# Kernel optimization log

Hardware: AMD Instinct MI355X
Metric: run time of the kernel (lower is better)

The kernel has to match this reference:

```python
import jax, jax.numpy as jnp
import numpy as np

BUCKET_BINS = np.array([0, 1, 2, 3, 4, 5, 7, 8, 15, 16, 31, 32, 63, 64], dtype=np.int32)
MAX_WINDOW = 8  # args.span_maximum_length


def _span_index_table(L):
    # Static enumeration of all spans of width 1..MAX_WINDOW (stride-1 unfold).
    starts, ends = [], []
    for w in range(1, min(L, MAX_WINDOW) + 1):
        s = np.arange(0, L - w + 1)
        starts.append(s)
        ends.append(s + w)
    return (np.concatenate(starts).astype(np.int32),
            np.concatenate(ends).astype(np.int32))


def _bucket(width):
    # index of last bin with width >= bin value
    return jnp.searchsorted(jnp.asarray(BUCKET_BINS), width, side='right') - 1


def _fnn(h, W1, b1, W2, b2, W3, b3):
    # Linear->ReLU->(Dropout: eval identity)->Linear->ReLU->Linear->Softmax
    h = jax.nn.relu(h @ W1 + b1)
    h = jax.nn.relu(h @ W2 + b2)
    return jax.nn.softmax(h @ W3 + b3, axis=-1)


def setup_inputs() -> dict:
    key = jax.random.key(0)
    ks = jax.random.split(key, 16)
    B, L, D = 8, 256, 768
    H, WD, DD = 1024, 25, 25
    span_dim = 2 * D + WD          # 1561
    pair_dim = 2 * span_dim + DD   # 3147
    f = jnp.float32

    def g(k, shape, scale):
        return jax.random.normal(k, shape, dtype=f) * scale

    return {
        'x': g(ks[0], (B, L, D), 1.0),
        'width_emb': g(ks[1], (len(BUCKET_BINS), WD), 0.02),
        'dist_emb': g(ks[2], (len(BUCKET_BINS), DD), 0.02),
        'Ws1': g(ks[3], (span_dim, H), 0.02), 'bs1': jnp.zeros((H,), f),
        'Ws2': g(ks[4], (H, H), 0.02), 'bs2': jnp.zeros((H,), f),
        'Ws3': g(ks[5], (H, 3), 0.02), 'bs3': jnp.zeros((3,), f),
        'Wp1': g(ks[6], (pair_dim, H), 0.02), 'bp1': jnp.zeros((H,), f),
        'Wp2': g(ks[7], (H, H), 0.02), 'bp2': jnp.zeros((H,), f),
        'Wp3': g(ks[8], (H, 4), 0.02), 'bp3': jnp.zeros((4,), f),
        'nz': 64,
    }


def reference(x, width_emb, dist_emb, Ws1, bs1, Ws2, bs2, Ws3, bs3,
              Wp1, bp1, Wp2, bp2, Wp3, bp3, nz):
    B, L, D = x.shape
    starts_np, ends_np = _span_index_table(L)
    starts = jnp.asarray(starts_np)
    ends = jnp.asarray(ends_np)

    # ---- SpanRepresentation: [start token, end token, width bucket emb] ----
    w_emb = width_emb[_bucket(ends - starts)]                     # [S, WD]
    spans = jnp.concatenate([
        x[:, starts_np, :],                                       # [B,S,D]
        x[:, ends_np - 1, :],                                     # [B,S,D]
        jnp.broadcast_to(w_emb, (B,) + w_emb.shape),              # [B,S,WD]
    ], axis=-1)                                                   # [B,S,span_dim]

    # ---- span_fnn + PrunedTargetOpinion (top-k on aspect/opinion probs) ----
    span_prob = _fnn(spans, Ws1, bs1, Ws2, bs2, Ws3, bs3)         # [B,S,3]
    _, t_idx = jax.lax.top_k(span_prob[:, :, 1], nz)              # aspect  [B,nz]
    _, o_idx = jax.lax.top_k(span_prob[:, :, 2], nz)              # opinion [B,nz]

    # ---- PairRepresentation: all target x opinion pairs ----
    t_rep = jnp.take_along_axis(spans, t_idx[:, :, None], axis=1) # [B,nz,sd]
    o_rep = jnp.take_along_axis(spans, o_idx[:, :, None], axis=1)
    ta, tb = starts[t_idx], ends[t_idx]                           # [B,nz]
    oc, od = starts[o_idx], ends[o_idx]
    # min_distance(a,b,c,d) = min(|b-c|, |a-d|)
    dist = jnp.minimum(jnp.abs(tb[:, :, None] - oc[:, None, :]),
                       jnp.abs(ta[:, :, None] - od[:, None, :]))  # [B,nz,nz]
    d_emb = dist_emb[_bucket(dist)]                               # [B,nz,nz,DD]
    sd = spans.shape[-1]
    pairs = jnp.concatenate([
        jnp.broadcast_to(t_rep[:, :, None, :], (B, nz, nz, sd)),
        jnp.broadcast_to(o_rep[:, None, :, :], (B, nz, nz, sd)),
        d_emb,
    ], axis=-1).reshape(B, nz * nz, 2 * sd + d_emb.shape[-1])     # [B,nz^2,pair_dim]

    pair_prob = _fnn(pairs, Wp1, bp1, Wp2, bp2, Wp3, bp3)         # [B,nz^2,4]
    return span_prob, pair_prob
```

## Files before the change

kernel.cpp:

```cpp
#include <hip/hip_runtime.h>
#include <cstdint>
#include <cstddef>

#define BATCH 8
#define SEQ   256
#define DIM   768
#define NSPAN 2020
#define HID   1024
#define NZ    64

typedef unsigned short u16;
typedef unsigned int   u32;
typedef unsigned long long u64;

typedef __bf16 bf16x8 __attribute__((ext_vector_type(8)));
typedef float  f32x4  __attribute__((ext_vector_type(4)));

__device__ __forceinline__ u16 f2bf(float f) {
    union { float f; u32 u; } x; x.f = f;
    u32 r = x.u + 0x7fffu + ((x.u >> 16) & 1u);
    return (u16)(r >> 16);
}
__device__ __forceinline__ float bf2f(u16 b) {
    union { u32 u; float f; } x; x.u = ((u32)b) << 16;
    return x.f;
}
__device__ __forceinline__ void splitbf(float v, u16& h, u16& l) {
    h = f2bf(v);
    l = f2bf(v - bf2f(h));
}

__device__ __forceinline__ void gld_lds16(const void* g, void* l) {
    __builtin_amdgcn_global_load_lds(
        (const __attribute__((address_space(1))) unsigned int*)g,
        (__attribute__((address_space(3))) unsigned int*)l, 16, 0, 0);
}

__device__ __forceinline__ void span_decode(int s, int& start, int& end, int& w) {
    int off = 0;
#pragma unroll
    for (int wi = 1; wi <= 8; ++wi) {
        int cnt = SEQ - wi + 1;
        if (s < off + cnt) { w = wi; start = s - off; end = start + wi; return; }
        off += cnt;
    }
    w = 8; start = 0; end = 8;
}

__device__ __forceinline__ int dbucket(int d) {
    int b = 0;
    b += (d >= 1);  b += (d >= 2);  b += (d >= 3);  b += (d >= 4);
    b += (d >= 5);  b += (d >= 7);  b += (d >= 8);  b += (d >= 15);
    b += (d >= 16); b += (d >= 31); b += (d >= 32); b += (d >= 63);
    b += (d >= 64);
    return b;
}

__device__ __forceinline__ void xcd_map(int L, int sft, int& bx, int& by) {
    int grp = L >> (3 + sft);
    int rem = L & ((1 << (3 + sft)) - 1);
    bx = rem >> 3;
    by = (grp << 3) | (rem & 7);
}

__global__ __launch_bounds__(256) void k_prep(
    const float* __restrict__ x,  u16* __restrict__ xh,   u16* __restrict__ xl,
    const float* __restrict__ wemb, const float* __restrict__ demb,
    const float* __restrict__ bs1, const float* __restrict__ bp1,
    float* __restrict__ wtabS, float* __restrict__ wtabPt,
    float* __restrict__ wtabPo, float* __restrict__ dtab,
    const float* __restrict__ Ws1, u16* __restrict__ W1Th, u16* __restrict__ W1Tl,
    const float* __restrict__ Ws2, u16* __restrict__ W2Th, u16* __restrict__ W2Tl,
    const float* __restrict__ Wp2, u16* __restrict__ Wp2T,
    const float* __restrict__ Wp1, u16* __restrict__ Wp1T4)
{
    __shared__ float tile[32][33];
    const int bid = blockIdx.x, tid = threadIdx.x;
    if (bid < 6144) {
        int i = bid * 256 + tid;
        u16 h, l; splitbf(x[i], h, l);
        xh[i] = h; xl[i] = l;
        return;
    }
    if (bid < 6296) {
        int t = bid - 6144;
        int row = t >> 2;
        int h = (t & 3) * 256 + tid;
        const int wb[8] = {1,2,3,4,5,5,6,7};
        if (row < 8) {
            int bk = wb[row];
            float acc = bs1[h];
            for (int j = 0; j < 25; ++j) acc = fmaf(wemb[bk*25+j], Ws1[(size_t)(1536+j)*HID + h], acc);
            wtabS[row*HID + h] = acc;
        } else if (row < 16) {
            int bk = wb[row-8];
            float acc = 0.f;
            for (int j = 0; j < 25; ++j) acc = fmaf(wemb[bk*25+j], Wp1[(size_t)(1536+j)*HID + h], acc);
            wtabPt[(row-8)*HID + h] = acc;
        } else if (row < 24) {
            int bk = wb[row-16];
            float acc = 0.f;
            for (int j = 0; j < 25; ++j) acc = fmaf(wemb[bk*25+j], Wp1[(size_t)(3097+j)*HID + h], acc);
            wtabPo[(row-16)*HID + h] = acc;
        } else {
            int tt = row - 24;
            float acc = bp1[h];
            for (int j = 0; j < 25; ++j) acc = fmaf(demb[tt*25+j], Wp1[(size_t)(3122+j)*HID + h], acc);
            dtab[tt*HID + h] = acc;
        }
        return;
    }
    const int tb = bid - 6296;
    const int tr = tid >> 3;
    const int tc4 = (tid & 7) * 4;
    int job, tk, tn, blk = 0;
    if (tb < 1536)      { job = 0; tk = tb % 24; tn = tb / 24; }
    else if (tb < 2560) { job = 1; int t = tb - 1536; tk = t & 31; tn = t >> 5; }
    else if (tb < 3584) { job = 2; int t = tb - 2560; tk = t & 31; tn = t >> 5; }
    else                { job = 3; int t = tb - 3584; blk = t / 768; int r = t - blk * 768; tk = r % 24; tn = r / 24; }
    const int k0 = tk * 32, n0 = tn * 32;

    int k = k0 + tr;
    float4 v;
    if (job == 0) {
        const float* s = (n0 < 1024) ? (Ws1 + (size_t)k * HID + n0)
                                     : (Ws1 + (size_t)(768 + k) * HID + (n0 - 1024));
        v = *(const float4*)(s + tc4);
    } else if (job == 1) {
        v = *(const float4*)(Ws2 + (size_t)k * HID + n0 + tc4);
    } else if (job == 2) {
        v = *(const float4*)(Wp2 + (size_t)k * HID + n0 + tc4);
    } else {
        const int roff[4] = {0, 768, 1561, 2329};
        v = *(const float4*)(Wp1 + (size_t)(roff[blk] + k) * HID + n0 + tc4);
    }
    tile[tr][tc4+0] = v.x; tile[tr][tc4+1] = v.y;
    tile[tr][tc4+2] = v.z; tile[tr][tc4+3] = v.w;
    __syncthreads();

    int nn = n0 + tr;
    float w0 = tile[tc4+0][tr], w1 = tile[tc4+1][tr];
    float w2 = tile[tc4+2][tr], w3 = tile[tc4+3][tr];
    if (job == 0) {
        size_t d = (size_t)nn * 768 + k0 + tc4;
        u16 h0,l0,h1,l1,h2,l2,h3,l3;
        splitbf(w0,h0,l0); splitbf(w1,h1,l1); splitbf(w2,h2,l2); splitbf(w3,h3,l3);
        *(uint2*)(W1Th + d) = make_uint2((u32)h0 | ((u32)h1 << 16), (u32)h2 | ((u32)h3 << 16));
        *(uint2*)(W1Tl + d) = make_uint2((u32)l0 | ((u32)l1 << 16), (u32)l2 | ((u32)l3 << 16));
    } else if (job == 1) {
        size_t d = (size_t)nn * 1024 + k0 + tc4;
        u16 h0,l0,h1,l1,h2,l2,h3,l3;
        splitbf(w0,h0,l0); splitbf(w1,h1,l1); splitbf(w2,h2,l2); splitbf(w3,h3,l3);
        *(uint2*)(W2Th + d) = make_uint2((u32)h0 | ((u32)h1 << 16), (u32)h2 | ((u32)h3 << 16));
        *(uint2*)(W2Tl + d) = make_uint2((u32)l0 | ((u32)l1 << 16), (u32)l2 | ((u32)l3 << 16));
    } else if (job == 2) {
        size_t d = (size_t)nn * 1024 + k0 + tc4;
        *(uint2*)(Wp2T + d) = make_uint2((u32)f2bf(w0) | ((u32)f2bf(w1) << 16),
                                         (u32)f2bf(w2) | ((u32)f2bf(w3) << 16));
    } else {
        size_t d = (size_t)blk * 786432 + (size_t)nn * 768 + k0 + tc4;
        *(uint2*)(Wp1T4 + d) = make_uint2((u32)f2bf(w0) | ((u32)f2bf(w1) << 16),
                                          (u32)f2bf(w2) | ((u32)f2bf(w3) << 16));
    }
}

__global__ __launch_bounds__(256) void k_gemm3bf(
    const u16* __restrict__ Ah, const u16* __restrict__ Al, int lda,
    const u16* __restrict__ BTh, const u16* __restrict__ BTl, int ldb,
    float* __restrict__ C, int ldc,
    int M, int K, int nby, int sft)
{
    int bx, by;
    xcd_map(blockIdx.x, sft, bx, by);
    if (by >= nby) return;
    __shared__ __align__(16) u16 sm[4 * 128 * 32];
    u16* sAh = sm;
    u16* sAl = sm + 4096;
    u16* sBh = sm + 8192;
    u16* sBl = sm + 12288;
    const int tid = threadIdx.x;
    const int bm = by * 128, bn = bx * 128;
    const int wave = tid >> 6, lane = tid & 63;
    const int wr = wave >> 1, wc = wave & 1;
    const int q = lane >> 4, tl = lane & 15;

    f32x4 zero = {0.f, 0.f, 0.f, 0.f};
    f32x4 acc[4][4];
#pragma unroll
    for (int i = 0; i < 4; ++i)
#pragma unroll
        for (int j = 0; j < 4; ++j) acc[i][j] = zero;

    const int srow = lane >> 2;
    const int scol = (lane & 3) * 8;
    int ra0 = bm + wave * 32 + srow;      if (ra0 >= M) ra0 = M - 1;
    int ra1 = bm + wave * 32 + 16 + srow; if (ra1 >= M) ra1 = M - 1;
    const int rb0 = bn + wave * 32 + srow;
    const int rb1 = bn + wave * 32 + 16 + srow;
    u16* dA0 = sAh + wave * 1024;  u16* dA1 = dA0 + 512;
    u16* dL0 = sAl + wave * 1024;  u16* dL1 = dL0 + 512;
    u16* dB0 = sBh + wave * 1024;  u16* dB1 = dB0 + 512;
    u16* dC0 = sBl + wave * 1024;  u16* dC1 = dC0 + 512;
    const u16* gA0 = Ah  + (size_t)ra0 * lda + scol;
    const u16* gA1 = Ah  + (size_t)ra1 * lda + scol;
    const u16* gL0 = Al  + (size_t)ra0 * lda + scol;
    const u16* gL1 = Al  + (size_t)ra1 * lda + scol;
    const u16* gB0 = BTh + (size_t)rb0 * ldb + scol;
    const u16* gB1 = BTh + (size_t)rb1 * ldb + scol;
    const u16* gC0 = BTl + (size_t)rb0 * ldb + scol;
    const u16* gC1 = BTl + (size_t)rb1 * ldb + scol;

    for (int k0 = 0; k0 < K; k0 += 32) {
        gld_lds16(gA0 + k0, dA0);
        gld_lds16(gA1 + k0, dA1);
        gld_lds16(gL0 + k0, dL0);
        gld_lds16(gL1 + k0, dL1);
        gld_lds16(gB0 + k0, dB0);
        gld_lds16(gB1 + k0, dB1);
        gld_lds16(gC0 + k0, dC0);
        gld_lds16(gC1 + k0, dC1);
        __syncthreads();
        bf16x8 ah[4], al[4], bh[4], bl[4];
#pragma unroll
        for (int t = 0; t < 4; ++t) {
            int arow = (wr*64 + t*16 + tl) * 32 + q*8;
            int brow = (wc*64 + t*16 + tl) * 32 + q*8;
            ah[t] = *(const bf16x8*)(&sAh[arow]);
            al[t] = *(const bf16x8*)(&sAl[arow]);
            bh[t] = *(const bf16x8*)(&sBh[brow]);
            bl[t] = *(const bf16x8*)(&sBl[brow]);
        }
#pragma unroll
        for (int ti = 0; ti < 4; ++ti)
#pragma unroll
            for (int tj = 0; tj < 4; ++tj) {
                acc[ti][tj] = __builtin_amdgcn_mfma_f32_16x16x32_bf16(ah[ti], bh[tj], acc[ti][tj], 0, 0, 0);
                acc[ti][tj] = __builtin_amdgcn_mfma_f32_16x16x32_bf16(al[ti], bh[tj], acc[ti][tj], 0, 0, 0);
                acc[ti][tj] = __builtin_amdgcn_mfma_f32_16x16x32_bf16(ah[ti], bl[tj], acc[ti][tj], 0, 0, 0);
            }
        __syncthreads();
    }
#pragma unroll
    for (int ti = 0; ti < 4; ++ti) {
#pragma unroll
        for (int tj = 0; tj < 4; ++tj) {
            int gcol = bn + wc*64 + tj*16 + tl;
#pragma unroll
            for (int r = 0; r < 4; ++r) {
                int grow = bm + wr*64 + ti*16 + q*4 + r;
                if (grow >= M) continue;
                C[(size_t)grow * ldc + gcol] = acc[ti][tj][r];
            }
        }
    }
}

#define MFB __builtin_amdgcn_mfma_f32_16x16x32_bf16
#define MFROW(i, A, B) \
    acc[i][0] = MFB(A, B[0], acc[i][0], 0, 0, 0); \
    acc[i][1] = MFB(A, B[1], acc[i][1], 0, 0, 0); \
    acc[i][2] = MFB(A, B[2], acc[i][2], 0, 0, 0); \
    acc[i][3] = MFB(A, B[3], acc[i][3], 0, 0, 0);

#define SPAN_PHASE(P, VMC) \
    { \
        bf16x8 ah0 = *(const bf16x8*)(smr + rA + (2*(P)+0)*512); \
        bf16x8 ah1 = *(const bf16x8*)(smr + rA + (2*(P)+1)*512); \
        bf16x8 al0 = *(const bf16x8*)(smr + rA + 8192 + (2*(P)+0)*512); \
        bf16x8 al1 = *(const bf16x8*)(smr + rA + 8192 + (2*(P)+1)*512); \
        if ((P) == 0) { \
            bh[0] = *(const bf16x8*)(smr + rB + 0*512); \
            bh[1] = *(const bf16x8*)(smr + rB + 1*512); \
            bh[2] = *(const bf16x8*)(smr + rB + 2*512); \
            bh[3] = *(const bf16x8*)(smr + rB + 3*512); \
            bl[0] = *(const bf16x8*)(smr + rB + 8192 + 0*512); \
            bl[1] = *(const bf16x8*)(smr + rB + 8192 + 1*512); \
            bl[2] = *(const bf16x8*)(smr + rB + 8192 + 2*512); \
            bl[3] = *(const bf16x8*)(smr + rB + 8192 + 3*512); \
        } \
        gld_lds16(gsrc[2*(P)+0] + kn, smw + ldst[2*(P)+0]); \
        gld_lds16(gsrc[2*(P)+1] + kn, smw + ldst[2*(P)+1]); \
        asm volatile("s_waitcnt vmcnt(" #VMC ")" ::: "memory"); \
        asm volatile("s_barrier" ::: "memory"); \
        __builtin_amdgcn_sched_barrier(0); \
        __builtin_amdgcn_s_setprio(1); \
        MFROW(2*(P)+0, ah0, bh) \
        MFROW(2*(P)+1, ah1, bh) \
        MFROW(2*(P)+0, al0, bh) \
        MFROW(2*(P)+1, al1, bh) \
        MFROW(2*(P)+0, ah0, bl) \
        MFROW(2*(P)+1, ah1, bl) \
        __builtin_amdgcn_s_setprio(0); \
        asm volatile("s_barrier" ::: "memory"); \
    }

__global__ __launch_bounds__(512, 2) void k_span_l2(
    const u16* __restrict__ Ah, const u16* __restrict__ Al,
    const u16* __restrict__ BTh, const u16* __restrict__ BTl,
    const float* __restrict__ bs2, const float* __restrict__ Ws3,
    float* __restrict__ part, int M)
{
    __shared__ __align__(16) u16 sm[65536];
    const int tid = threadIdx.x;
    const int swz = (blockIdx.x & 7) * 32 + (blockIdx.x >> 3);
    const int by = swz >> 2, bx = swz & 3;
    const int bm = by * 256, bn = bx * 256;
    const int wave = tid >> 6, lane = tid & 63;
    const int wm = wave >> 2, wn = wave & 3;
    const int tl = lane & 15, q8 = lane >> 4;

    const int sr  = lane >> 2;
    const int scs = lane & 3;
    const int scl = scs ^ ((sr >> 1) & 3);
    const u16* gsrc[8];
    u32 ldst[8];
#pragma unroll
    for (int c = 0; c < 4; ++c) {
        int arr  = 2 + (c >> 1);
        int half = c & 1;
        int sb   = wave;
        int row  = bn + half * 128 + sb * 16 + sr;
        const u16* base = (arr == 2) ? BTh : BTl;
        gsrc[c] = base + (size_t)row * HID + scl * 8;
        ldst[c] = arr * 8192 + half * 4096 + sb * 512;
    }
#pragma unroll
    for (int p = 0; p < 4; ++p) {
        int arr  = wave >> 2;
        int half = (wave >> 1) & 1;
        int sb   = 2 * p + (wave & 1);
        int row  = bm + half * 128 + sb * 16 + sr;
        if (row >= M) row = M - 1;
        const u16* base = arr ? Al : Ah;
        gsrc[4 + p] = base + (size_t)row * HID + scl * 8;
        ldst[4 + p] = arr * 8192 + half * 4096 + sb * 512;
    }
    const int cpr = q8 ^ ((tl >> 1) & 3);
    const u32 lof = (u32)(tl * 32 + cpr * 8);
    const u32 rA  = (u32)(wm * 4096) + lof;
    const u32 rB  = 16384u + (u32)((wn >> 1) * 4096 + (wn & 1) * 2048) + lof;

    f32x4 zero = {0.f, 0.f, 0.f, 0.f};
    f32x4 acc[8][4];
#pragma unroll
    for (int i = 0; i < 8; ++i)
#pragma unroll
        for (int j = 0; j < 4; ++j) acc[i][j] = zero;

#pragma unroll
    for (int c = 0; c < 8; ++c) gld_lds16(gsrc[c], sm + ldst[c]);
    asm volatile("s_waitcnt vmcnt(3)" ::: "memory");
    asm volatile("s_barrier" ::: "memory");

    bf16x8 bh[4], bl[4];
    for (int t = 0; t < 32; ++t) {
        const u16* smr = sm + ((t & 1) ? 32768u : 0u);
        u16*       smw = sm + ((t & 1) ? 0u : 32768u);
        const int  kn  = (t + 1) * 32;
        SPAN_PHASE(0, 4)
        SPAN_PHASE(1, 5)
        SPAN_PHASE(2, 6)
        SPAN_PHASE(3, 3)
    }

    const int slot = bx * 4 + wn;
#pragma unroll
    for (int fm = 0; fm < 8; ++fm) {
#pragma unroll
        for (int r = 0; r < 4; ++r) {
            int grow = bm + wm * 128 + fm * 16 + q8 * 4 + r;
            float l0 = 0.f, l1 = 0.f, l2 = 0.f;
#pragma unroll
            for (int fn = 0; fn < 4; ++fn) {
                int gcol = bn + wn * 64 + fn * 16 + tl;
                float v = fmaxf(acc[fm][fn][r] + bs2[gcol], 0.f);
                const float* w3 = Ws3 + gcol * 3;
                l0 = fmaf(v, w3[0], l0);
                l1 = fmaf(v, w3[1], l1);
                l2 = fmaf(v, w3[2], l2);
            }
#pragma unroll
            for (int off = 8; off > 0; off >>= 1) {
                l0 += __shfl_down(l0, off, 16);
                l1 += __shfl_down(l1, off, 16);
                l2 += __shfl_down(l2, off, 16);
            }
            if (tl == 0 && grow < M) {
                float* dst = part + ((size_t)grow * 16 + slot) * 3;
                dst[0] = l0; dst[1] = l1; dst[2] = l2;
            }
        }
    }
    asm volatile("s_waitcnt vmcnt(0)" ::: "memory");
}

__global__ __launch_bounds__(256) void k_pairL1(
    const u16* __restrict__ xh, const u16* __restrict__ Wp1T4,
    float* __restrict__ TO2, const int* __restrict__ toks)
{
    __shared__ __align__(16) u16 sm[2 * 64 * 32];
    u16* sA = sm;
    u16* sB = sm + 2048;
    const int tid = threadIdx.x;
    const int bid = blockIdx.x;
    const int p = bid >> 8;
    const int bx = bid & 15, by = (bid >> 4) & 15;
    const int bm = by * 64, bn = bx * 64;
    const int wave = tid >> 6, lane = tid & 63;
    const int wr = wave >> 1, wc = wave & 1;
    const int q = lane >> 4, tl = lane & 15;
    const bool isO = bm >= 512;

    f32x4 zero = {0.f, 0.f, 0.f, 0.f};
    f32x4 acc[2][2];
#pragma unroll
    for (int i = 0; i < 2; ++i)
#pragma unroll
        for (int j = 0; j < 2; ++j) acc[i][j] = zero;

    const int srow = tid >> 2;
    const int scol = (tid & 3) * 8;
    u16* dA = sA + wave * 512;
    u16* dB = sB + wave * 512;

    int arow = toks[bm + srow + p * 1024];
    const u16* gA = xh + (size_t)arow * DIM + scol;
    const u16* gB = Wp1T4 + ((size_t)((isO ? 2 : 0) + p) * 1024 + bn + srow) * DIM + scol;
    for (int k0 = 0; k0 < DIM; k0 += 32) {
        gld_lds16(gA + k0, dA);
        gld_lds16(gB + k0, dB);
        __syncthreads();
        bf16x8 af[2], bf[2];
#pragma unroll
        for (int t = 0; t < 2; ++t) {
            af[t] = *(const bf16x8*)(&sA[(wr*32 + t*16 + tl) * 32 + q*8]);
            bf[t] = *(const bf16x8*)(&sB[(wc*32 + t*16 + tl) * 32 + q*8]);
        }
#pragma unroll
        for (int ti = 0; ti < 2; ++ti)
#pragma unroll
            for (int tj = 0; tj < 2; ++tj)
                acc[ti][tj] = __builtin_amdgcn_mfma_f32_16x16x32_bf16(af[ti], bf[tj], acc[ti][tj], 0, 0, 0);
        __syncthreads();
    }
    float* dstb = TO2 + (size_t)p * 1024 * HID;
#pragma unroll
    for (int ti = 0; ti < 2; ++ti) {
#pragma unroll
        for (int tj = 0; tj < 2; ++tj) {
            int gcol = bn + wc*32 + tj*16 + tl;
#pragma unroll
            for (int r = 0; r < 4; ++r) {
                int grow = bm + wr*32 + ti*16 + q*4 + r;
                dstb[(size_t)grow * HID + gcol] = acc[ti][tj][r];
            }
        }
    }
}

__global__ __launch_bounds__(256) void k_build_h1s(
    const float* __restrict__ XALL, const float* __restrict__ wtabS,
    u16* __restrict__ h1h, u16* __restrict__ h1l)
{
    int r = blockIdx.x;
    int b = r / NSPAN, s = r - b * NSPAN;
    int st, en, w; span_decode(s, st, en, w);
    const float4* xs = (const float4*)(XALL + (size_t)(b*SEQ + st) * 2048);
    const float4* xe = (const float4*)(XALL + (size_t)(b*SEQ + en - 1) * 2048 + 1024);
    const float4* wt = (const float4*)(wtabS + (size_t)(w-1) * HID);
    int t = threadIdx.x;
    float4 a = xs[t], bz = xe[t], c = wt[t];
    float v0 = fmaxf(a.x + bz.x + c.x, 0.f);
    float v1 = fmaxf(a.y + bz.y + c.y, 0.f);
    float v2 = fmaxf(a.z + bz.z + c.z, 0.f);
    float v3 = fmaxf(a.w + bz.w + c.w, 0.f);
    u16 h0,l0,h1,l1,h2,l2,h3,l3;
    splitbf(v0,h0,l0); splitbf(v1,h1,l1); splitbf(v2,h2,l2); splitbf(v3,h3,l3);
    size_t base = (size_t)r * HID + t * 4;
    *(uint2*)(h1h + base) = make_uint2((u32)h0 | ((u32)h1 << 16), (u32)h2 | ((u32)h3 << 16));
    *(uint2*)(h1l + base) = make_uint2((u32)l0 | ((u32)l1 << 16), (u32)l2 | ((u32)l3 << 16));
}

__global__ __launch_bounds__(256) void k_topk(
    const float* __restrict__ partS, const float* __restrict__ bs3,
    float* __restrict__ out, int* __restrict__ t_idx, int* __restrict__ o_idx,
    int* __restrict__ toks)
{
    int b = blockIdx.x >> 1;
    int head = 1 + (blockIdx.x & 1);
    int* outp = (head == 1 ? t_idx : o_idx) + b * NZ;
    __shared__ u64 keys[2048];
    int tid = threadIdx.x;
#pragma unroll
    for (int ii = 0; ii < 8; ++ii) {
        int s = tid + ii * 256;
        u32 fb = 0;
        if (s < NSPAN) {
            const float* p = partS + (size_t)(b * NSPAN + s) * 48;
            float s0 = bs3[0], s1 = bs3[1], s2 = bs3[2];
#pragma unroll
            for (int t = 0; t < 16; ++t) {
                s0 += p[t*3]; s1 += p[t*3+1]; s2 += p[t*3+2];
            }
            float m = fmaxf(s0, fmaxf(s1, s2));
            float e0 = expf(s0 - m), e1 = expf(s1 - m), e2 = expf(s2 - m);
            float inv = 1.f / (e0 + e1 + e2);
            float p0 = e0 * inv, p1 = e1 * inv, p2 = e2 * inv;
            float* o = out + (size_t)(b * NSPAN + s) * 3;
            o[0] = p0; o[1] = p1; o[2] = p2;
            union { float f; u32 u; } x;
            x.f = (head == 1) ? p1 : p2;
            fb = x.u;
        }
        keys[s] = ((u64)fb << 32) | (u64)(0xFFFFFFFFu - (u32)s);
    }
    __syncthreads();
    for (int k = 2; k <= 2048; k <<= 1) {
        for (int j = k >> 1; j > 0; j >>= 1) {
#pragma unroll
            for (int ii = 0; ii < 8; ++ii) {
                int i = tid + ii * 256;
                int ixj = i ^ j;
                if (ixj > i) {
                    u64 a = keys[i], c = keys[ixj];
                    bool desc = (i & k) == 0;
                    bool wrong = desc ? (a < c) : (a > c);
                    if (wrong) { keys[i] = c; keys[ixj] = a; }
                }
            }
            __syncthreads();
        }
    }
    if (tid < NZ) {
        u64 key = keys[tid];
        int fi = (int)(0xFFFFFFFFu - (u32)(key & 0xFFFFFFFFu));
        if (fi < 0 || fi >= NSPAN) fi = 0;
        outp[tid] = fi;
        int st, en, w; span_decode(fi, st, en, w);
        int base = (head == 1 ? 0 : 512) + b * NZ + tid;
        toks[base] = b * SEQ + st;
        toks[1024 + base] = b * SEQ + en - 1;
    }
}

__global__ __launch_bounds__(256) void k_build_h1p(
    const float* __restrict__ TO2, const int* __restrict__ t_idx, const int* __restrict__ o_idx,
    const float* __restrict__ wtabPt, const float* __restrict__ wtabPo,
    const float* __restrict__ dtab, u16* __restrict__ h1p)
{
    __shared__ float Ts[8][HID];
    __shared__ float Os[4][HID];
    const int bid = blockIdx.x;
    const int b = bid >> 7;
    const int it = (bid >> 4) & 7;
    const int jt = bid & 15;
    const int i0 = it * 8, j0 = jt * 4;
    const int tid = threadIdx.x;
    const int k4 = tid * 4;
    const size_t PS = (size_t)1024 * HID;

    int tinfo[8][2];
    int oinfo[4][2];
#pragma unroll
    for (int r = 0; r < 8; ++r) {
        int i = i0 + r;
        int ts = t_idx[b*64 + i];
        int ta, tb, wt; span_decode(ts, ta, tb, wt);
        tinfo[r][0] = ta; tinfo[r][1] = tb;
        float4 t0 = *(const float4*)(TO2 + (size_t)(b*64 + i) * HID + k4);
        float4 t1 = *(const float4*)(TO2 + PS + (size_t)(b*64 + i) * HID + k4);
        float4 pp = *(const float4*)(wtabPt + (size_t)(wt-1) * HID + k4);
        Ts[r][k4+0] = t0.x + t1.x + pp.x;
        Ts[r][k4+1] = t0.y + t1.y + pp.y;
        Ts[r][k4+2] = t0.z + t1.z + pp.z;
        Ts[r][k4+3] = t0.w + t1.w + pp.w;
    }
#pragma unroll
    for (int r = 0; r < 4; ++r) {
        int j = j0 + r;
        int os = o_idx[b*64 + j];
        int oc, od, wo; span_decode(os, oc, od, wo);
        oinfo[r][0] = oc; oinfo[r][1] = od;
        float4 o0 = *(const float4*)(TO2 + (size_t)(512 + b*64 + j) * HID + k4);
        float4 o1 = *(const float4*)(TO2 + PS + (size_t)(512 + b*64 + j) * HID + k4);
        float4 qq = *(const float4*)(wtabPo + (size_t)(wo-1) * HID + k4);
        Os[r][k4+0] = o0.x + o1.x + qq.x;
        Os[r][k4+1] = o0.y + o1.y + qq.y;
        Os[r][k4+2] = o0.z + o1.z + qq.z;
        Os[r][k4+3] = o0.w + o1.w + qq.w;
    }
    __syncthreads();

#pragma unroll
    for (int ri = 0; ri < 8; ++ri) {
#pragma unroll
        for (int rj = 0; rj < 4; ++rj) {
            int ta = tinfo[ri][0], tb = tinfo[ri][1];
            int oc = oinfo[rj][0], od = oinfo[rj][1];
            int d1 = tb - oc; d1 = d1 < 0 ? -d1 : d1;
            int d2 = ta - od; d2 = d2 < 0 ? -d2 : d2;
            int dist = d1 < d2 ? d1 : d2;
            int db = dbucket(dist);
            const float4 dd = *(const float4*)(dtab + (size_t)db * HID + k4);
            float vx = fmaxf(Ts[ri][k4+0] + Os[rj][k4+0] + dd.x, 0.f);
            float vy = fmaxf(Ts[ri][k4+1] + Os[rj][k4+1] + dd.y, 0.f);
            float vz = fmaxf(Ts[ri][k4+2] + Os[rj][k4+2] + dd.z, 0.f);
            float vw = fmaxf(Ts[ri][k4+3] + Os[rj][k4+3] + dd.w, 0.f);
            u32 p0 = (u32)f2bf(vx) | ((u32)f2bf(vy) << 16);
            u32 p1 = (u32)f2bf(vz) | ((u32)f2bf(vw) << 16);
            int row = b * 4096 + (i0 + ri) * 64 + (j0 + rj);
            *(uint2*)(h1p + (size_t)row * HID + k4) = make_uint2(p0, p1);
        }
    }
}

#define PAIR_PHASE(P, VMC) \
    { \
        bf16x8 a00 = *(const bf16x8*)(smr + rA + ((2*(P)+0)*2+0)*512); \
        bf16x8 a01 = *(const bf16x8*)(smr + rA + ((2*(P)+0)*2+1)*512); \
        bf16x8 a10 = *(const bf16x8*)(smr + rA + ((2*(P)+1)*2+0)*512); \
        bf16x8 a11 = *(const bf16x8*)(smr + rA + ((2*(P)+1)*2+1)*512); \
        if ((P) == 0) { \
            b0[0] = *(const bf16x8*)(smr + rB + 0*512); \
            b1[0] = *(const bf16x8*)(smr + rB + 1*512); \
            b0[1] = *(const bf16x8*)(smr + rB + 2*512); \
            b1[1] = *(const bf16x8*)(smr + rB + 3*512); \
            b0[2] = *(const bf16x8*)(smr + rB + 4*512); \
            b1[2] = *(const bf16x8*)(smr + rB + 5*512); \
            b0[3] = *(const bf16x8*)(smr + rB + 6*512); \
            b1[3] = *(const bf16x8*)(smr + rB + 7*512); \
        } \
        gld_lds16(gsrc[2*(P)+0] + kn, smw + ldst[2*(P)+0]); \
        gld_lds16(gsrc[2*(P)+1] + kn, smw + ldst[2*(P)+1]); \
        asm volatile("s_waitcnt vmcnt(" #VMC ")" ::: "memory"); \
        asm volatile("s_barrier" ::: "memory"); \
        __builtin_amdgcn_sched_barrier(0); \
        __builtin_amdgcn_s_setprio(1); \
        MFROW(2*(P)+0, a00, b0) \
        MFROW(2*(P)+1, a10, b0) \
        MFROW(2*(P)+0, a01, b1) \
        MFROW(2*(P)+1, a11, b1) \
        __builtin_amdgcn_s_setprio(0); \
        asm volatile("s_barrier" ::: "memory"); \
    }

__global__ __launch_bounds__(512, 2) void k_pair_l2(
    const u16* __restrict__ Abf, const u16* __restrict__ BT,
    const float* __restrict__ bp2, const float* __restrict__ Wp3,
    float* __restrict__ part)
{
    __shared__ __align__(16) u16 sm[65536];
    const int tid = threadIdx.x;
    const int swz = (blockIdx.x & 7) * 64 + (blockIdx.x >> 3);
    const int by = swz >> 2, bx = swz & 3;
    const int bm = by * 256, bn = bx * 256;
    const int wave = tid >> 6, lane = tid & 63;
    const int wm = wave >> 2, wn = wave & 3;
    const int tl = lane & 15, q8 = lane >> 4;

    const int sr  = lane >> 2;
    const int scs = lane & 3;
    const int scl = scs ^ ((sr >> 1) & 3);
    const u16* gsrc[8];
    u32 ldst[8];
#pragma unroll
    for (int c = 0; c < 4; ++c) {
        int half = c >> 1;
        int sb   = (c & 1) * 8 + wave;
        int row  = bn + half * 128 + (sb >> 1) * 16 + sr;
        gsrc[c] = BT + (size_t)row * HID + (sb & 1) * 32 + scl * 8;
        ldst[c] = 16384 + half * 8192 + sb * 512;
    }
#pragma unroll
    for (int p = 0; p < 4; ++p) {
        int half = wave >> 2;
        int sb   = 4 * p + (wave & 3);
        int row  = bm + half * 128 + (sb >> 1) * 16 + sr;
        gsrc[4 + p] = Abf + (size_t)row * HID + (sb & 1) * 32 + scl * 8;
        ldst[4 + p] = half * 8192 + sb * 512;
    }
    const int cpr = q8 ^ ((tl >> 1) & 3);
    const u32 lof = (u32)(tl * 32 + cpr * 8);
    const u32 rA  = (u32)(wm * 8192) + lof;
    const u32 rB  = 16384u + (u32)((wn >> 1) * 8192 + (wn & 1) * 4096) + lof;

    f32x4 zero = {0.f, 0.f, 0.f, 0.f};
    f32x4 acc[8][4];
#pragma unroll
    for (int i = 0; i < 8; ++i)
#pragma unroll
        for (int j = 0; j < 4; ++j) acc[i][j] = zero;

#pragma unroll
    for (int c = 0; c < 8; ++c) gld_lds16(gsrc[c], sm + ldst[c]);
    asm volatile("s_waitcnt vmcnt(3)" ::: "memory");
    asm volatile("s_barrier" ::: "memory");

    bf16x8 b0[4], b1[4];
    for (int t = 0; t < 16; ++t) {
        const u16* smr = sm + ((t & 1) ? 32768u : 0u);
        u16*       smw = sm + ((t & 1) ? 0u : 32768u);
        const int  kn  = (t + 1) * 64;
        PAIR_PHASE(0, 4)
        PAIR_PHASE(1, 5)
        PAIR_PHASE(2, 6)
        PAIR_PHASE(3, 3)
    }

    const int slot = bx * 4 + wn;
#pragma unroll
    for (int fm = 0; fm < 8; ++fm) {
#pragma unroll
        for (int r = 0; r < 4; ++r) {
            int grow = bm + wm * 128 + fm * 16 + q8 * 4 + r;
            float l0 = 0.f, l1 = 0.f, l2 = 0.f, l3 = 0.f;
#pragma unroll
            for (int fn = 0; fn < 4; ++fn) {
                int gcol = bn + wn * 64 + fn * 16 + tl;
                float v = fmaxf(acc[fm][fn][r] + bp2[gcol], 0.f);
                const float4 w = *(const float4*)(Wp3 + gcol * 4);
                l0 = fmaf(v, w.x, l0); l1 = fmaf(v, w.y, l1);
                l2 = fmaf(v, w.z, l2); l3 = fmaf(v, w.w, l3);
            }
#pragma unroll
            for (int off = 8; off > 0; off >>= 1) {
                l0 += __shfl_down(l0, off, 16);
                l1 += __shfl_down(l1, off, 16);
                l2 += __shfl_down(l2, off, 16);
                l3 += __shfl_down(l3, off, 16);
            }
            if (tl == 0) {
                float* dst = part + ((size_t)grow * 16 + slot) * 4;
                dst[0] = l0; dst[1] = l1; dst[2] = l2; dst[3] = l3;
            }
        }
    }
    asm volatile("s_waitcnt vmcnt(0)" ::: "memory");
}

__global__ __launch_bounds__(256) void k_pair_red(
    const float* __restrict__ part, const float* __restrict__ bp3,
    float* __restrict__ out)
{
    int r = blockIdx.x * 256 + threadIdx.x;
    const float4* p = (const float4*)(part + (size_t)r * 64);
    float s0 = bp3[0], s1 = bp3[1], s2 = bp3[2], s3 = bp3[3];
#pragma unroll
    for (int t = 0; t < 16; ++t) {
        float4 v = p[t];
        s0 += v.x; s1 += v.y; s2 += v.z; s3 += v.w;
    }
    float m = fmaxf(fmaxf(s0, s1), fmaxf(s2, s3));
    float e0 = expf(s0 - m), e1 = expf(s1 - m), e2 = expf(s2 - m), e3 = expf(s3 - m);
    float inv = 1.f / (e0 + e1 + e2 + e3);
    float* o = out + (size_t)r * 4;
    o[0] = e0 * inv; o[1] = e1 * inv; o[2] = e2 * inv; o[3] = e3 * inv;
}

extern "C" void kernel_launch(void* const* d_in, const int* in_sizes, int n_in,
                              void* d_out, int out_size, void* d_ws, size_t ws_size,
                              hipStream_t stream)
{
    const float* x    = (const float*)d_in[0];
    const float* wemb = (const float*)d_in[1];
    const float* demb = (const float*)d_in[2];
    const float* Ws1  = (const float*)d_in[3];
    const float* bs1  = (const float*)d_in[4];
    const float* Ws2  = (const float*)d_in[5];
    const float* bs2  = (const float*)d_in[6];
    const float* Ws3  = (const float*)d_in[7];
    const float* bs3  = (const float*)d_in[8];
    const float* Wp1  = (const float*)d_in[9];
    const float* bp1  = (const float*)d_in[10];
    const float* Wp2  = (const float*)d_in[11];
    const float* bp2  = (const float*)d_in[12];
    const float* Wp3  = (const float*)d_in[13];
    const float* bp3  = (const float*)d_in[14];
    float* out = (float*)d_out;
    char* ws = (char*)d_ws;

    const size_t RSZ = (size_t)32768 * HID * 2;
    size_t off = 0;
    auto alloc = [&](size_t bytes) -> void* {
        void* p = ws + off;
        off += (bytes + 255) & ~(size_t)255;
        return p;
    };
    char* R1 = (char*)alloc(RSZ);
    char* R2 = (char*)alloc(RSZ);
    u16*   h1h  = (u16*)R1;
    u16*   h1l  = (u16*)(R1 + (size_t)16160 * HID * 2);
    float* XALL = (float*)R2;
    u16*   xl   = (u16*)(R2 + (16u << 20));
    u16*   W1Th = (u16*)(R2 + (19u << 20));
    u16*   W1Tl = (u16*)(R2 + (22u << 20));
    u16*   h1p  = (u16*)R2;
    u16*   xh     = (u16*)alloc((size_t)2048 * DIM * 2);
    float* TO2    = (float*)alloc((size_t)2 * 1024 * HID * 4);
    float* partS  = (float*)alloc((size_t)16160 * 16 * 3 * 4);
    float* partP  = (float*)alloc((size_t)32768 * 16 * 4 * 4);
    u16*   W2Th   = (u16*)alloc((size_t)1024 * 1024 * 2);
    u16*   W2Tl   = (u16*)alloc((size_t)1024 * 1024 * 2);
    u16*   Wp2T   = (u16*)alloc((size_t)1024 * 1024 * 2);
    u16*   Wp1T4  = (u16*)alloc((size_t)4 * 1024 * 768 * 2);
    float* wtabS  = (float*)alloc(8 * HID * 4);
    float* wtabPt = (float*)alloc(8 * HID * 4);
    float* wtabPo = (float*)alloc(8 * HID * 4);
    float* dtab   = (float*)alloc(14 * HID * 4);
    int*   t_idx  = (int*)alloc(BATCH * NZ * 4);
    int*   o_idx  = (int*)alloc(BATCH * NZ * 4);
    int*   toks   = (int*)alloc(2048 * 4);
    (void)ws_size; (void)in_sizes; (void)n_in; (void)out_size;

    k_prep<<<12952, 256, 0, stream>>>(x, xh, xl, wemb, demb, bs1, bp1,
                                      wtabS, wtabPt, wtabPo, dtab,
                                      Ws1, W1Th, W1Tl, Ws2, W2Th, W2Tl,
                                      Wp2, Wp2T, Wp1, Wp1T4);

    k_gemm3bf<<<256, 256, 0, stream>>>(xh, xl, 768, W1Th, W1Tl, 768,
                                       XALL, 2048, 2048, 768, 16, 4);
    k_build_h1s<<<16160, 256, 0, stream>>>(XALL, wtabS, h1h, h1l);
    k_span_l2<<<256, 512, 0, stream>>>(h1h, h1l, W2Th, W2Tl, bs2, Ws3, partS, 16160);
    k_topk<<<16, 256, 0, stream>>>(partS, bs3, out, t_idx, o_idx, toks);
    k_pairL1<<<512, 256, 0, stream>>>(xh, Wp1T4, TO2, toks);
    k_build_h1p<<<1024, 256, 0, stream>>>(TO2, t_idx, o_idx, wtabPt, wtabPo, dtab, h1p);
    k_pair_l2<<<512, 512, 0, stream>>>(h1p, Wp2T, bp2, Wp3, partP);
    k_pair_red<<<128, 256, 0, stream>>>(partP, bp3, out + 48480);
}
```

Before: 438.5 us.

## Retile pair layer-2 GEMM to 256x128 tiles and rebalance span prefetch

The pair layer-2 GEMM moves from 256x256 tiles with K-step 64 to 256x128 tiles with K-step 32. Shared memory drops to 48 KB and launch bounds rise to four blocks per CU, doubling the grid to 1024 blocks. The partial-logit buffer grows to 32 slots per row and is aliased into the now-dead R1 region, and the reduction kernel sums 32 partials. The span layer-2 loop redistributes its eight global-to-LDS loads across phases (3/2/2/1) with adjusted vmcnt waits. Smaller tiles trade lower arithmetic intensity per byte loaded for higher occupancy and better latency hiding.

```diff
diff --git a/kernel.cpp b/kernel.cpp
--- a/kernel.cpp
+++ b/kernel.cpp
@@ -261,8 +261,11 @@
     acc[i][1] = MFB(A, B[1], acc[i][1], 0, 0, 0); \
     acc[i][2] = MFB(A, B[2], acc[i][2], 0, 0, 0); \
     acc[i][3] = MFB(A, B[3], acc[i][3], 0, 0, 0);
-
-#define SPAN_PHASE(P, VMC) \
+#define MFROW2(i, A, B) \
+    acc[i][0] = MFB(A, B[0], acc[i][0], 0, 0, 0); \
+    acc[i][1] = MFB(A, B[1], acc[i][1], 0, 0, 0);
+
+#define SPAN_PHASE(P, VMC, GLDS) \
     { \
         bf16x8 ah0 = *(const bf16x8*)(smr + rA + (2*(P)+0)*512); \
         bf16x8 ah1 = *(const bf16x8*)(smr + rA + (2*(P)+1)*512); \
@@ -278,8 +281,7 @@
             bl[2] = *(const bf16x8*)(smr + rB + 8192 + 2*512); \
             bl[3] = *(const bf16x8*)(smr + rB + 8192 + 3*512); \
         } \
-        gld_lds16(gsrc[2*(P)+0] + kn, smw + ldst[2*(P)+0]); \
-        gld_lds16(gsrc[2*(P)+1] + kn, smw + ldst[2*(P)+1]); \
+        GLDS \
         asm volatile("s_waitcnt vmcnt(" #VMC ")" ::: "memory"); \
         asm volatile("s_barrier" ::: "memory"); \
         __builtin_amdgcn_sched_barrier(0); \
@@ -357,10 +359,18 @@
         const u16* smr = sm + ((t & 1) ? 32768u : 0u);
         u16*       smw = sm + ((t & 1) ? 0u : 32768u);
         const int  kn  = (t + 1) * 32;
-        SPAN_PHASE(0, 4)
-        SPAN_PHASE(1, 5)
-        SPAN_PHASE(2, 6)
-        SPAN_PHASE(3, 3)
+        SPAN_PHASE(0, 5,
+            gld_lds16(gsrc[0] + kn, smw + ldst[0]);
+            gld_lds16(gsrc[1] + kn, smw + ldst[1]);
+            gld_lds16(gsrc[2] + kn, smw + ldst[2]);)
+        SPAN_PHASE(1, 6,
+            gld_lds16(gsrc[3] + kn, smw + ldst[3]);
+            gld_lds16(gsrc[4] + kn, smw + ldst[4]);)
+        SPAN_PHASE(2, 7,
+            gld_lds16(gsrc[5] + kn, smw + ldst[5]);
+            gld_lds16(gsrc[6] + kn, smw + ldst[6]);)
+        SPAN_PHASE(3, 3,
+            gld_lds16(gsrc[7] + kn, smw + ldst[7]);)
     }
 
     const int slot = bx * 4 + wn;
@@ -614,46 +624,39 @@
     }
 }
 
-#define PAIR_PHASE(P, VMC) \
+#define PAIR4_PHASE(FM0, VMC, GLDS) \
     { \
-        bf16x8 a00 = *(const bf16x8*)(smr + rA + ((2*(P)+0)*2+0)*512); \
-        bf16x8 a01 = *(const bf16x8*)(smr + rA + ((2*(P)+0)*2+1)*512); \
-        bf16x8 a10 = *(const bf16x8*)(smr + rA + ((2*(P)+1)*2+0)*512); \
-        bf16x8 a11 = *(const bf16x8*)(smr + rA + ((2*(P)+1)*2+1)*512); \
-        if ((P) == 0) { \
-            b0[0] = *(const bf16x8*)(smr + rB + 0*512); \
-            b1[0] = *(const bf16x8*)(smr + rB + 1*512); \
-            b0[1] = *(const bf16x8*)(smr + rB + 2*512); \
-            b1[1] = *(const bf16x8*)(smr + rB + 3*512); \
-            b0[2] = *(const bf16x8*)(smr + rB + 4*512); \
-            b1[2] = *(const bf16x8*)(smr + rB + 5*512); \
-            b0[3] = *(const bf16x8*)(smr + rB + 6*512); \
-            b1[3] = *(const bf16x8*)(smr + rB + 7*512); \
+        bf16x8 a0 = *(const bf16x8*)(smr + rA + ((FM0)+0)*512); \
+        bf16x8 a1 = *(const bf16x8*)(smr + rA + ((FM0)+1)*512); \
+        bf16x8 a2 = *(const bf16x8*)(smr + rA + ((FM0)+2)*512); \
+        bf16x8 a3 = *(const bf16x8*)(smr + rA + ((FM0)+3)*512); \
+        if ((FM0) == 0) { \
+            bb[0] = *(const bf16x8*)(smr + rB + 0*512); \
+            bb[1] = *(const bf16x8*)(smr + rB + 1*512); \
         } \
-        gld_lds16(gsrc[2*(P)+0] + kn, smw + ldst[2*(P)+0]); \
-        gld_lds16(gsrc[2*(P)+1] + kn, smw + ldst[2*(P)+1]); \
+        GLDS \
         asm volatile("s_waitcnt vmcnt(" #VMC ")" ::: "memory"); \
         asm volatile("s_barrier" ::: "memory"); \
         __builtin_amdgcn_sched_barrier(0); \
         __builtin_amdgcn_s_setprio(1); \
-        MFROW(2*(P)+0, a00, b0) \
-        MFROW(2*(P)+1, a10, b0) \
-        MFROW(2*(P)+0, a01, b1) \
-        MFROW(2*(P)+1, a11, b1) \
+        MFROW2((FM0)+0, a0, bb) \
+        MFROW2((FM0)+1, a1, bb) \
+        MFROW2((FM0)+2, a2, bb) \
+        MFROW2((FM0)+3, a3, bb) \
         __builtin_amdgcn_s_setprio(0); \
         asm volatile("s_barrier" ::: "memory"); \
     }
 
-__global__ __launch_bounds__(512, 2) void k_pair_l2(
+__global__ __launch_bounds__(512, 4) void k_pair_l2(
     const u16* __restrict__ Abf, const u16* __restrict__ BT,
     const float* __restrict__ bp2, const float* __restrict__ Wp3,
     float* __restrict__ part)
 {
-    __shared__ __align__(16) u16 sm[65536];
+    __shared__ __align__(16) u16 sm[24576];
     const int tid = threadIdx.x;
-    const int swz = (blockIdx.x & 7) * 64 + (blockIdx.x >> 3);
-    const int by = swz >> 2, bx = swz & 3;
-    const int bm = by * 256, bn = bx * 256;
+    const int swz = (blockIdx.x & 7) * 128 + (blockIdx.x >> 3);
+    const int by = swz >> 3, bx = swz & 7;
+    const int bm = by * 256, bn = bx * 128;
     const int wave = tid >> 6, lane = tid & 63;
     const int wm = wave >> 2, wn = wave & 3;
     const int tl = lane & 15, q8 = lane >> 4;
@@ -661,50 +664,48 @@
     const int sr  = lane >> 2;
     const int scs = lane & 3;
     const int scl = scs ^ ((sr >> 1) & 3);
-    const u16* gsrc[8];
-    u32 ldst[8];
-#pragma unroll
-    for (int c = 0; c < 4; ++c) {
-        int half = c >> 1;
-        int sb   = (c & 1) * 8 + wave;
-        int row  = bn + half * 128 + (sb >> 1) * 16 + sr;
-        gsrc[c] = BT + (size_t)row * HID + (sb & 1) * 32 + scl * 8;
-        ldst[c] = 16384 + half * 8192 + sb * 512;
-    }
-#pragma unroll
-    for (int p = 0; p < 4; ++p) {
-        int half = wave >> 2;
-        int sb   = 4 * p + (wave & 3);
-        int row  = bm + half * 128 + (sb >> 1) * 16 + sr;
-        gsrc[4 + p] = Abf + (size_t)row * HID + (sb & 1) * 32 + scl * 8;
-        ldst[4 + p] = half * 8192 + sb * 512;
+    const u16* gsrc[3];
+    u32 ldst[3];
+    {
+        int rowB = bn + wave * 16 + sr;
+        gsrc[0] = BT + (size_t)rowB * HID + scl * 8;
+        ldst[0] = 8192 + wave * 512;
+        int ps1 = (wave & 3) + (wave >> 2) * 8;
+        int rowA1 = bm + ps1 * 16 + sr;
+        gsrc[1] = Abf + (size_t)rowA1 * HID + scl * 8;
+        ldst[1] = ps1 * 512;
+        int ps2 = ps1 + 4;
+        int rowA2 = bm + ps2 * 16 + sr;
+        gsrc[2] = Abf + (size_t)rowA2 * HID + scl * 8;
+        ldst[2] = ps2 * 512;
     }
     const int cpr = q8 ^ ((tl >> 1) & 3);
     const u32 lof = (u32)(tl * 32 + cpr * 8);
-    const u32 rA  = (u32)(wm * 8192) + lof;
-    const u32 rB  = 16384u + (u32)((wn >> 1) * 8192 + (wn & 1) * 4096) + lof;
+    const u32 rA  = (u32)(wm * 4096) + lof;
+    const u32 rB  = 8192u + (u32)(wn * 1024) + lof;
 
     f32x4 zero = {0.f, 0.f, 0.f, 0.f};
-    f32x4 acc[8][4];
+    f32x4 acc[8][2];
 #pragma unroll
     for (int i = 0; i < 8; ++i)
 #pragma unroll
-        for (int j = 0; j < 4; ++j) acc[i][j] = zero;
-
-#pragma unroll
-    for (int c = 0; c < 8; ++c) gld_lds16(gsrc[c], sm + ldst[c]);
-    asm volatile("s_waitcnt vmcnt(3)" ::: "memory");
+        for (int j = 0; j < 2; ++j) acc[i][j] = zero;
+
+#pragma unroll
+    for (int c = 0; c < 3; ++c) gld_lds16(gsrc[c], sm + ldst[c]);
+    asm volatile("s_waitcnt vmcnt(1)" ::: "memory");
     asm volatile("s_barrier" ::: "memory");
 
-    bf16x8 b0[4], b1[4];
-    for (int t = 0; t < 16; ++t) {
-        const u16* smr = sm + ((t & 1) ? 32768u : 0u);
-        u16*       smw = sm + ((t & 1) ? 0u : 32768u);
-        const int  kn  = (t + 1) * 64;
-        PAIR_PHASE(0, 4)
-        PAIR_PHASE(1, 5)
-        PAIR_PHASE(2, 6)
-        PAIR_PHASE(3, 3)
+    bf16x8 bb[2];
+    for (int t = 0; t < 32; ++t) {
+        const u16* smr = sm + ((t & 1) ? 12288u : 0u);
+        u16*       smw = sm + ((t & 1) ? 0u : 12288u);
+        const int  kn  = (t + 1) * 32;
+        PAIR4_PHASE(0, 2,
+            gld_lds16(gsrc[0] + kn, smw + ldst[0]);
+            gld_lds16(gsrc[1] + kn, smw + ldst[1]);)
+        PAIR4_PHASE(4, 1,
+            gld_lds16(gsrc[2] + kn, smw + ldst[2]);)
     }
 
     const int slot = bx * 4 + wn;
@@ -715,8 +716,8 @@
             int grow = bm + wm * 128 + fm * 16 + q8 * 4 + r;
             float l0 = 0.f, l1 = 0.f, l2 = 0.f, l3 = 0.f;
 #pragma unroll
-            for (int fn = 0; fn < 4; ++fn) {
-                int gcol = bn + wn * 64 + fn * 16 + tl;
+            for (int fn = 0; fn < 2; ++fn) {
+                int gcol = bn + wn * 32 + fn * 16 + tl;
                 float v = fmaxf(acc[fm][fn][r] + bp2[gcol], 0.f);
                 const float4 w = *(const float4*)(Wp3 + gcol * 4);
                 l0 = fmaf(v, w.x, l0); l1 = fmaf(v, w.y, l1);
@@ -730,7 +731,7 @@
                 l3 += __shfl_down(l3, off, 16);
             }
             if (tl == 0) {
-                float* dst = part + ((size_t)grow * 16 + slot) * 4;
+                float* dst = part + ((size_t)grow * 32 + slot) * 4;
                 dst[0] = l0; dst[1] = l1; dst[2] = l2; dst[3] = l3;
             }
         }
@@ -743,10 +744,10 @@
     float* __restrict__ out)
 {
     int r = blockIdx.x * 256 + threadIdx.x;
-    const float4* p = (const float4*)(part + (size_t)r * 64);
+    const float4* p = (const float4*)(part + (size_t)r * 128);
     float s0 = bp3[0], s1 = bp3[1], s2 = bp3[2], s3 = bp3[3];
 #pragma unroll
-    for (int t = 0; t < 16; ++t) {
+    for (int t = 0; t < 32; ++t) {
         float4 v = p[t];
         s0 += v.x; s1 += v.y; s2 += v.z; s3 += v.w;
     }
@@ -790,6 +791,7 @@
     char* R2 = (char*)alloc(RSZ);
     u16*   h1h  = (u16*)R1;
     u16*   h1l  = (u16*)(R1 + (size_t)16160 * HID * 2);
+    float* partP = (float*)R1;
     float* XALL = (float*)R2;
     u16*   xl   = (u16*)(R2 + (16u << 20));
     u16*   W1Th = (u16*)(R2 + (19u << 20));
@@ -798,7 +800,7 @@
     u16*   xh     = (u16*)alloc((size_t)2048 * DIM * 2);
     float* TO2    = (float*)alloc((size_t)2 * 1024 * HID * 4);
     float* partS  = (float*)alloc((size_t)16160 * 16 * 3 * 4);
-    float* partP  = (float*)alloc((size_t)32768 * 16 * 4 * 4);
+    float* partP_unused = (float*)alloc((size_t)32768 * 16 * 4 * 4);
     u16*   W2Th   = (u16*)alloc((size_t)1024 * 1024 * 2);
     u16*   W2Tl   = (u16*)alloc((size_t)1024 * 1024 * 2);
     u16*   Wp2T   = (u16*)alloc((size_t)1024 * 1024 * 2);
@@ -810,7 +812,7 @@
     int*   t_idx  = (int*)alloc(BATCH * NZ * 4);
     int*   o_idx  = (int*)alloc(BATCH * NZ * 4);
     int*   toks   = (int*)alloc(2048 * 4);
-    (void)ws_size; (void)in_sizes; (void)n_in; (void)out_size;
+    (void)ws_size; (void)in_sizes; (void)n_in; (void)out_size; (void)partP_unused;
 
     k_prep<<<12952, 256, 0, stream>>>(x, xh, xl, wemb, demb, bs1, bp1,
                                       wtabS, wtabPt, wtabPo, dtab,
@@ -824,6 +826,6 @@
     k_topk<<<16, 256, 0, stream>>>(partS, bs3, out, t_idx, o_idx, toks);
     k_pairL1<<<512, 256, 0, stream>>>(xh, Wp1T4, TO2, toks);
     k_build_h1p<<<1024, 256, 0, stream>>>(TO2, t_idx, o_idx, wtabPt, wtabPo, dtab, h1p);
-    k_pair_l2<<<512, 512, 0, stream>>>(h1p, Wp2T, bp2, Wp3, partP);
+    k_pair_l2<<<1024, 512, 0, stream>>>(h1p, Wp2T, bp2, Wp3, partP);
     k_pair_red<<<128, 256, 0, stream>>>(partP, bp3, out + 48480);
 }
```

Result: slower. 457.6 us (+4.3%).
